# Performance work log

Hardware: AMD Instinct MI355X
Metric: run time of the kernel (lower is better)

The kernel has to match this reference:

```python
import jax, jax.numpy as jnp
import numpy as np

DIM = 256
TIME_DIM = 64
BETA = 0.5
VOCAB = 150
B, L = 2048, 128


def setup_inputs() -> dict:
    key = jax.random.key(0)
    ks = jax.random.split(key, 9)
    u = lambda k, shape: jax.random.uniform(k, shape, jnp.float32, -0.1, 0.1)
    return {
        "out": jax.random.normal(ks[0], (B, L, DIM), jnp.float32),
        "hn": jax.random.normal(ks[1], (B, DIM), jnp.float32),
        "pos_ind": jax.random.randint(ks[2], (B, L), 0, VOCAB),
        "rel_dt": jax.random.randint(ks[3], (B, L), 0, VOCAB),
        "abs_dt": jnp.zeros((B, L), jnp.float32),
        "pos_emb_w": u(ks[4], (VOCAB, TIME_DIM)),
        "rel_emb_w": u(ks[5], (VOCAB, TIME_DIM)),
        "Wk": u(ks[6], (DIM, DIM)),   # fc_k.weight: y = x @ Wk.T
        "Wq": u(ks[7], (DIM, DIM)),   # fc_q.weight
        "Wrp": u(ks[8], (1, 2 * TIME_DIM)),  # fc_rp.weight
    }


def reference(out, hn, pos_ind, rel_dt, abs_dt, pos_emb_w, rel_emb_w, Wk, Wq, Wrp):
    temperature = np.sqrt(DIM * 1.0).astype(np.float32)
    pad_mask = pos_ind == 0                      # [B, L]
    pos_e = pos_emb_w[pos_ind]                   # [B, L, T]
    rel_e = rel_emb_w[rel_dt]                    # [B, L, T]
    attn_k = jnp.einsum('bld,ed->ble', out, Wk)  # fc_k(out)
    attn_q = jnp.einsum('bd,ed->be', hn, Wq)     # fc_q(hn)
    attn_0 = jnp.einsum('bld,bd->bl', attn_k, attn_q) / temperature
    attn_1 = jnp.einsum('blt,ot->bl', jnp.concatenate([rel_e, pos_e], -1), Wrp)
    attn = attn_0 + BETA * attn_1
    attn = jnp.where(pad_mask, -jnp.inf, attn)
    attn = jax.nn.softmax(attn, axis=1)
    return jnp.einsum('bl,bld->bd', attn, out)   # [B, D]
```

## Files before the change

### kernel.cpp

```cpp
#include <hip/hip_runtime.h>

#define DIM 256
#define L_ 128
#define TD 64
#define NVOCAB 150
#define NB 2048

__device__ __forceinline__ float dot4(float4 a, float4 b) {
    return fmaf(a.x, b.x, fmaf(a.y, b.y, fmaf(a.z, b.z, a.w * b.w)));
}

__global__ __launch_bounds__(256) void prep_kernel(
    const float* __restrict__ Wk, const float* __restrict__ Wq,
    const float* __restrict__ Wrp,
    const float* __restrict__ rel_emb_w, const float* __restrict__ pos_emb_w,
    float* __restrict__ M, float* __restrict__ rel_s, float* __restrict__ pos_s)
{
    if (blockIdx.x == DIM) {
        int v = threadIdx.x;
        if (v < NVOCAB) {
            float sr = 0.f, sp = 0.f;
#pragma unroll 8
            for (int j = 0; j < TD; ++j) {
                sr = fmaf(rel_emb_w[v * TD + j], Wrp[j], sr);
                sp = fmaf(pos_emb_w[v * TD + j], Wrp[TD + j], sp);
            }
            rel_s[v] = 0.5f * sr;
            pos_s[v] = 0.5f * sp;
        }
        return;
    }
    int cc = blockIdx.x;
    int d  = threadIdx.x;
    float a0 = 0.f, a1 = 0.f, a2 = 0.f, a3 = 0.f;
#pragma unroll 8
    for (int e = 0; e < DIM; e += 4) {
        a0 = fmaf(Wq[(e + 0) * DIM + cc], Wk[(e + 0) * DIM + d], a0);
        a1 = fmaf(Wq[(e + 1) * DIM + cc], Wk[(e + 1) * DIM + d], a1);
        a2 = fmaf(Wq[(e + 2) * DIM + cc], Wk[(e + 2) * DIM + d], a2);
        a3 = fmaf(Wq[(e + 3) * DIM + cc], Wk[(e + 3) * DIM + d], a3);
    }
    M[cc * DIM + d] = (a0 + a1 + a2 + a3) * (1.0f / 16.0f);
}

__global__ __launch_bounds__(256) void qk_bias_kernel(
    const float* __restrict__ hn, const float* __restrict__ M,
    const int* __restrict__ pos_ind, const int* __restrict__ rel_dt,
    const float* __restrict__ rel_s, const float* __restrict__ pos_s,
    float* __restrict__ qk, float* __restrict__ bias_g)
{
    const int t = threadIdx.x;
    if (blockIdx.x >= NB / 8) {
        int idx = (blockIdx.x - NB / 8) * 256 + t;
        int pi = pos_ind[idx];
        int rd = rel_dt[idx];
        bias_g[idx] = (pi == 0) ? -1e30f : (rel_s[rd] + pos_s[pi]);
        return;
    }
    __shared__ float hn_s[8][DIM];
    const int r0 = blockIdx.x * 8;
#pragma unroll
    for (int i = 0; i < 8; ++i)
        hn_s[i][t] = hn[(size_t)(r0 + i) * DIM + t];
    __syncthreads();
    float acc[8] = {0.f, 0.f, 0.f, 0.f, 0.f, 0.f, 0.f, 0.f};
#pragma unroll 8
    for (int c = 0; c < DIM; ++c) {
        float m = M[c * DIM + t];
#pragma unroll
        for (int r = 0; r < 8; ++r)
            acc[r] = fmaf(hn_s[r][c], m, acc[r]);
    }
#pragma unroll
    for (int r = 0; r < 8; ++r)
        qk[(size_t)(r0 + r) * DIM + t] = acc[r];
}

__global__ __launch_bounds__(512, 4) void attn_main(
    const float* __restrict__ outp, const float* __restrict__ qk,
    const float* __restrict__ bias_g, float* __restrict__ y)
{
    const int b    = blockIdx.x;
    const int t    = threadIdx.x;
    const int w    = t >> 6;
    const int lane = t & 63;
    const int g    = lane >> 4;
    const int c    = lane & 15;
    const int grp  = (w << 2) | g;

    __shared__ float dG[32];
    __shared__ float red[32][DIM];

    const float4* __restrict__ src = (const float4*)outp + (size_t)b * (L_ * 64);
    const int r0   = (w << 4) | g;
    const int base = r0 * 64 + c;

    float4 v[16];
#pragma unroll
    for (int k = 0; k < 4; ++k)
#pragma unroll
        for (int j = 0; j < 4; ++j)
            v[k * 4 + j] = src[base + k * 256 + j * 16];

    const float4* __restrict__ qp = (const float4*)qk + (size_t)b * 64;
    float4 q[4];
#pragma unroll
    for (int j = 0; j < 4; ++j) q[j] = qp[c + j * 16];
    const float* __restrict__ bp = bias_g + (size_t)b * L_ + r0;
    float bi[4];
#pragma unroll
    for (int k = 0; k < 4; ++k) bi[k] = bp[4 * k];

    float lg[4];
#pragma unroll
    for (int k = 0; k < 4; ++k) {
        float p = dot4(v[k * 4 + 0], q[0]) + dot4(v[k * 4 + 1], q[1]) +
                  dot4(v[k * 4 + 2], q[2]) + dot4(v[k * 4 + 3], q[3]);
        p += __shfl_xor(p, 1);
        p += __shfl_xor(p, 2);
        p += __shfl_xor(p, 4);
        p += __shfl_xor(p, 8);
        lg[k] = p + bi[k];
    }

    float we[4];
    float d = 0.f;
#pragma unroll
    for (int k = 0; k < 4; ++k) { we[k] = __expf(lg[k]); d += we[k]; }

    float4 o[4];
#pragma unroll
    for (int j = 0; j < 4; ++j) o[j] = make_float4(0.f, 0.f, 0.f, 0.f);
#pragma unroll
    for (int k = 0; k < 4; ++k)
#pragma unroll
        for (int j = 0; j < 4; ++j) {
            o[j].x = fmaf(we[k], v[k * 4 + j].x, o[j].x);
            o[j].y = fmaf(we[k], v[k * 4 + j].y, o[j].y);
            o[j].z = fmaf(we[k], v[k * 4 + j].z, o[j].z);
            o[j].w = fmaf(we[k], v[k * 4 + j].w, o[j].w);
        }

    if (c == 0) dG[grp] = d;
    float4* rw = (float4*)(&red[grp][0]);
#pragma unroll
    for (int j = 0; j < 4; ++j) rw[c + j * 16] = o[j];
    __syncthreads();

    if (t < DIM) {
        float s = 0.f;
#pragma unroll
        for (int gg = 0; gg < 32; ++gg) s += red[gg][t];
        float D = 0.f;
#pragma unroll
        for (int gg = 0; gg < 32; ++gg) D += dG[gg];
        y[(size_t)b * DIM + t] = s / D;
    }
}

extern "C" void kernel_launch(void* const* d_in, const int* in_sizes, int n_in,
                              void* d_out, int out_size, void* d_ws, size_t ws_size,
                              hipStream_t stream)
{
    const float* out_t     = (const float*)d_in[0];
    const float* hn        = (const float*)d_in[1];
    const int*   pos_ind   = (const int*)  d_in[2];
    const int*   rel_dt    = (const int*)  d_in[3];
    const float* pos_emb_w = (const float*)d_in[5];
    const float* rel_emb_w = (const float*)d_in[6];
    const float* Wk        = (const float*)d_in[7];
    const float* Wq        = (const float*)d_in[8];
    const float* Wrp       = (const float*)d_in[9];

    float* y = (float*)d_out;

    float* M      = (float*)d_ws;
    float* qk     = M + DIM * DIM;
    float* rel_s  = qk + (size_t)NB * DIM;
    float* pos_s  = rel_s + 256;
    float* bias_g = pos_s + 256;

    prep_kernel<<<DIM + 1, 256, 0, stream>>>(Wk, Wq, Wrp, rel_emb_w, pos_emb_w,
                                             M, rel_s, pos_s);
    qk_bias_kernel<<<NB / 8 + (NB * L_) / 256, 256, 0, stream>>>(
        hn, M, pos_ind, rel_dt, rel_s, pos_s, qk, bias_g);
    attn_main<<<NB, 512, 0, stream>>>(out_t, qk, bias_g, y);
}
```

Measured before the change: 78.69 us.

## Assign one wavefront per batch row with double-buffered streaming over rows

Replaces the 512-thread-per-batch attention kernel with one 64-lane wavefront per batch element, four batches per block. Each wave streams the 128 rows with two register buffers, overlapping loads with the dot, exp and accumulate of the previous rows. The final reduction uses cross-lane shuffles instead of shared memory and __syncthreads. This cuts shared-memory traffic and block-level synchronisation. In exchange each wave has far more serial work and fewer loads in flight per batch, so memory-level parallelism now depends on occupancy.

```diff
diff --git a/kernel.cpp b/kernel.cpp
--- a/kernel.cpp
+++ b/kernel.cpp
@@ -76,85 +76,89 @@
         qk[(size_t)(r0 + r) * DIM + t] = acc[r];
 }
 
-__global__ __launch_bounds__(512, 4) void attn_main(
+__global__ __launch_bounds__(256) void attn_wave(
     const float* __restrict__ outp, const float* __restrict__ qk,
     const float* __restrict__ bias_g, float* __restrict__ y)
 {
-    const int b    = blockIdx.x;
-    const int t    = threadIdx.x;
-    const int w    = t >> 6;
-    const int lane = t & 63;
+    const int w    = threadIdx.x >> 6;
+    const int lane = threadIdx.x & 63;
     const int g    = lane >> 4;
     const int c    = lane & 15;
-    const int grp  = (w << 2) | g;
-
-    __shared__ float dG[32];
-    __shared__ float red[32][DIM];
+    const int b    = (blockIdx.x << 2) | w;
 
     const float4* __restrict__ src = (const float4*)outp + (size_t)b * (L_ * 64);
-    const int r0   = (w << 4) | g;
-    const int base = r0 * 64 + c;
+    const float4* __restrict__ qp  = (const float4*)qk + (size_t)b * 64;
+    const float*  __restrict__ bp  = bias_g + (size_t)b * L_;
 
-    float4 v[16];
-#pragma unroll
-    for (int k = 0; k < 4; ++k)
-#pragma unroll
-        for (int j = 0; j < 4; ++j)
-            v[k * 4 + j] = src[base + k * 256 + j * 16];
-
-    const float4* __restrict__ qp = (const float4*)qk + (size_t)b * 64;
     float4 q[4];
 #pragma unroll
-    for (int j = 0; j < 4; ++j) q[j] = qp[c + j * 16];
-    const float* __restrict__ bp = bias_g + (size_t)b * L_ + r0;
-    float bi[4];
-#pragma unroll
-    for (int k = 0; k < 4; ++k) bi[k] = bp[4 * k];
-
-    float lg[4];
-#pragma unroll
-    for (int k = 0; k < 4; ++k) {
-        float p = dot4(v[k * 4 + 0], q[0]) + dot4(v[k * 4 + 1], q[1]) +
-                  dot4(v[k * 4 + 2], q[2]) + dot4(v[k * 4 + 3], q[3]);
-        p += __shfl_xor(p, 1);
-        p += __shfl_xor(p, 2);
-        p += __shfl_xor(p, 4);
-        p += __shfl_xor(p, 8);
-        lg[k] = p + bi[k];
-    }
-
-    float we[4];
-    float d = 0.f;
-#pragma unroll
-    for (int k = 0; k < 4; ++k) { we[k] = __expf(lg[k]); d += we[k]; }
+    for (int j = 0; j < 4; ++j) q[j] = qp[j * 16 + c];
 
     float4 o[4];
 #pragma unroll
     for (int j = 0; j < 4; ++j) o[j] = make_float4(0.f, 0.f, 0.f, 0.f);
+    float d = 0.f;
+
+    float4 va[4], vb[4];
+    float biA, biB;
+
+#define LOADV(BUF, ROW)                                            \
+    do {                                                           \
+        _Pragma("unroll")                                          \
+        for (int j = 0; j < 4; ++j)                                \
+            BUF[j] = src[(ROW) * 64 + j * 16 + c];                 \
+    } while (0)
+
+#define PROC(BUF, BI)                                              \
+    do {                                                           \
+        float p = dot4(BUF[0], q[0]) + dot4(BUF[1], q[1]) +        \
+                  dot4(BUF[2], q[2]) + dot4(BUF[3], q[3]);         \
+        p += __shfl_xor(p, 1);                                     \
+        p += __shfl_xor(p, 2);                                     \
+        p += __shfl_xor(p, 4);                                     \
+        p += __shfl_xor(p, 8);                                     \
+        float we = __expf(p + (BI));                               \
+        d += we;                                                   \
+        _Pragma("unroll")                                          \
+        for (int j = 0; j < 4; ++j) {                              \
+            o[j].x = fmaf(we, BUF[j].x, o[j].x);                   \
+            o[j].y = fmaf(we, BUF[j].y, o[j].y);                   \
+            o[j].z = fmaf(we, BUF[j].z, o[j].z);                   \
+            o[j].w = fmaf(we, BUF[j].w, o[j].w);                   \
+        }                                                          \
+    } while (0)
+
+    LOADV(va, g);         biA = bp[g];
+    LOADV(vb, 4 + g);     biB = bp[4 + g];
+
+    for (int rb = 0; rb < L_ - 8; rb += 8) {
+        PROC(va, biA);
+        LOADV(va, rb + 8 + g);   biA = bp[rb + 8 + g];
+        PROC(vb, biB);
+        LOADV(vb, rb + 12 + g);  biB = bp[rb + 12 + g];
+    }
+    PROC(va, biA);
+    PROC(vb, biB);
+#undef LOADV
+#undef PROC
+
 #pragma unroll
-    for (int k = 0; k < 4; ++k)
+    for (int j = 0; j < 4; ++j) {
+        o[j].x += __shfl_xor(o[j].x, 16); o[j].y += __shfl_xor(o[j].y, 16);
+        o[j].z += __shfl_xor(o[j].z, 16); o[j].w += __shfl_xor(o[j].w, 16);
+        o[j].x += __shfl_xor(o[j].x, 32); o[j].y += __shfl_xor(o[j].y, 32);
+        o[j].z += __shfl_xor(o[j].z, 32); o[j].w += __shfl_xor(o[j].w, 32);
+    }
+    d += __shfl_xor(d, 16);
+    d += __shfl_xor(d, 32);
+
+    const float inv = 1.0f / d;
+    if (lane < 16) {
+        float4* __restrict__ yo = (float4*)(y + (size_t)b * DIM);
 #pragma unroll
-        for (int j = 0; j < 4; ++j) {
-            o[j].x = fmaf(we[k], v[k * 4 + j].x, o[j].x);
-            o[j].y = fmaf(we[k], v[k * 4 + j].y, o[j].y);
-            o[j].z = fmaf(we[k], v[k * 4 + j].z, o[j].z);
-            o[j].w = fmaf(we[k], v[k * 4 + j].w, o[j].w);
-        }
-
-    if (c == 0) dG[grp] = d;
-    float4* rw = (float4*)(&red[grp][0]);
-#pragma unroll
-    for (int j = 0; j < 4; ++j) rw[c + j * 16] = o[j];
-    __syncthreads();
-
-    if (t < DIM) {
-        float s = 0.f;
-#pragma unroll
-        for (int gg = 0; gg < 32; ++gg) s += red[gg][t];
-        float D = 0.f;
-#pragma unroll
-        for (int gg = 0; gg < 32; ++gg) D += dG[gg];
-        y[(size_t)b * DIM + t] = s / D;
+        for (int j = 0; j < 4; ++j)
+            yo[j * 16 + c] = make_float4(o[j].x * inv, o[j].y * inv,
+                                         o[j].z * inv, o[j].w * inv);
     }
 }
 
@@ -184,5 +188,5 @@
                                              M, rel_s, pos_s);
     qk_bias_kernel<<<NB / 8 + (NB * L_) / 256, 256, 0, stream>>>(
         hn, M, pos_ind, rel_dt, rel_s, pos_s, qk, bias_g);
-    attn_main<<<NB, 512, 0, stream>>>(out_t, qk, bias_g, y);
+    attn_wave<<<NB / 4, 256, 0, stream>>>(out_t, qk, bias_g, y);
 }
```

Result: slower. 81.98 us (+4.2%).
